# Performance work log

Measured on AMD Instinct MI355X. Metric: run time of the kernel, lower is better.

Reference implementation:

```python
import jax, jax.numpy as jnp
import numpy as np

B, T, D = 4, 2048, 1024
H = 16
HD = D // H  # 64


def setup_inputs() -> dict:
    key = jax.random.key(0)
    k1, k2, k3 = jax.random.split(key, 3)
    x = jax.random.normal(k1, (B, T, D), dtype=jnp.float32)
    w_qkv = jax.random.normal(k2, (D, 3 * D), dtype=jnp.float32) * (1.0 / np.sqrt(D))
    w_out = jax.random.normal(k3, (D, D), dtype=jnp.float32) * (1.0 / np.sqrt(D))
    return {"x": x, "w_qkv": w_qkv, "w_out": w_out}


def reference(x, w_qkv, w_out):
    b, t, c = x.shape
    qkv = x @ w_qkv  # [B,T,3D]
    q, k, v = jnp.split(qkv, 3, axis=-1)

    def heads(u):
        return u.reshape(b, t, H, HD).transpose(0, 2, 1, 3)  # [B,H,T,HD]

    q, k, v = heads(q), heads(k), heads(v)
    scale = 1.0 / np.sqrt(HD).astype(np.float32)
    attn = jnp.einsum('bhqd,bhkd->bhqk', q, k) * scale  # [B,H,T,T]
    causal = jnp.tril(jnp.ones((t, t), dtype=bool))
    attn = jnp.where(causal[None, None, :, :], attn, -jnp.inf)
    attn = jax.nn.softmax(attn, axis=-1)
    y = jnp.einsum('bhqk,bhkd->bhqd', attn, v)  # [B,H,T,HD]
    y = y.transpose(0, 2, 1, 3).reshape(b, t, c)
    return y @ w_out
```

## Files before the change

kernel.cpp:

```cpp
#include <hip/hip_runtime.h>
#include <hip/hip_bf16.h>
#include <stdint.h>

#define B_    4
#define T_    2048
#define D_    1024
#define H_    16
#define HD_   64
#define ROWS_ (B_ * T_)
#define NQKV_ (3 * D_)

typedef __attribute__((ext_vector_type(8))) short bf16x8;
typedef __attribute__((ext_vector_type(4))) float f32x4;

__device__ __forceinline__ unsigned short f2bf(float f) {
    union { float f; uint32_t u; } v; v.f = f;
    uint32_t u = v.u;
    return (unsigned short)((u + 0x7FFFu + ((u >> 16) & 1u)) >> 16);
}

__device__ __forceinline__ uint32_t pack2_rtz(float a, float b) {
    union { float f; uint32_t u; } x, y; x.f = a; y.f = b;
    return (x.u >> 16) | (y.u & 0xFFFF0000u);
}

__device__ __forceinline__ void glds16(const unsigned short* g, unsigned short* l) {
    __builtin_amdgcn_global_load_lds(
        (const __attribute__((address_space(1))) void*)g,
        (__attribute__((address_space(3))) void*)l, 16, 0, 0);
}

__global__ void cvt_bf16_kernel(const float* __restrict__ in,
                                unsigned short* __restrict__ out, int n8) {
    int i = blockIdx.x * blockDim.x + threadIdx.x;
    if (i >= n8) return;
    float4 a = ((const float4*)in)[2 * i];
    float4 b = ((const float4*)in)[2 * i + 1];
    union { bf16x8 v; unsigned short s[8]; } o;
    o.s[0] = f2bf(a.x); o.s[1] = f2bf(a.y); o.s[2] = f2bf(a.z); o.s[3] = f2bf(a.w);
    o.s[4] = f2bf(b.x); o.s[5] = f2bf(b.y); o.s[6] = f2bf(b.z); o.s[7] = f2bf(b.w);
    ((bf16x8*)out)[i] = o.v;
}

__global__ __launch_bounds__(256) void tcvt2_kernel(const float* __restrict__ wqkv,
                                                    const float* __restrict__ wout,
                                                    unsigned short* __restrict__ oqkv,
                                                    unsigned short* __restrict__ oout,
                                                    float scale) {
    __shared__ float tile[64 * 65];
    const int t = threadIdx.x;
    const bool second = blockIdx.x >= 48;
    const float* in = second ? wout : wqkv;
    unsigned short* out = second ? oout : oqkv;
    const int N = second ? 1024 : 3072;
    const int ncut = second ? 0 : 1024;
    const int n0 = (second ? (blockIdx.x - 48) : blockIdx.x) * 64;
    const int k0 = blockIdx.y * 64;
    const int K = 1024;
#pragma unroll
    for (int it = 0; it < 4; ++it) {
        int id = it * 256 + t;
        int r = id >> 4, c = (id & 15) * 4;
        float4 v = *(const float4*)&in[(size_t)(k0 + r) * N + n0 + c];
        tile[r * 65 + c + 0] = v.x; tile[r * 65 + c + 1] = v.y;
        tile[r * 65 + c + 2] = v.z; tile[r * 65 + c + 3] = v.w;
    }
    __syncthreads();
#pragma unroll
    for (int it = 0; it < 2; ++it) {
        int id = it * 256 + t;
        int n = id >> 3, kc = (id & 7) * 8;
        float sc = (n0 + n < ncut) ? scale : 1.0f;
        union { bf16x8 v; unsigned short s[8]; } o;
#pragma unroll
        for (int i = 0; i < 8; ++i) o.s[i] = f2bf(tile[(kc + i) * 65 + n] * sc);
        *(bf16x8*)&out[(size_t)(n0 + n) * K + k0 + kc] = o.v;
    }
}

template<int OUT_BF16, int VSPLIT>
__global__ __launch_bounds__(256) void gemm128_kernel(
    const unsigned short* __restrict__ A,
    const unsigned short* __restrict__ Bt,
    void* __restrict__ Cp, int M, int K, int ldC,
    unsigned short* __restrict__ vt)
{
    __shared__ __align__(16) unsigned short As[128 * 64];
    __shared__ __align__(16) unsigned short Bs[128 * 64];

    const int t = threadIdx.x, w = t >> 6, lane = t & 63;
    const int wm = w >> 1, wn = w & 1;
    const int lm = lane & 15, lq = lane >> 4;
    const int m0 = blockIdx.y * 128, n0 = blockIdx.x * 128;

    f32x4 acc[4][4];
#pragma unroll
    for (int i = 0; i < 4; i++)
#pragma unroll
        for (int j = 0; j < 4; j++) acc[i][j] = (f32x4){0.f, 0.f, 0.f, 0.f};

    const unsigned short* Ap[4];
    const unsigned short* Bp[4];
#pragma unroll
    for (int s = 0; s < 4; s++) {
        int id = s * 256 + t;
        int row = id >> 3, gch = (id & 7) ^ (row & 7);
        Ap[s] = A  + (size_t)(m0 + row) * K + gch * 8;
        Bp[s] = Bt + (size_t)(n0 + row) * K + gch * 8;
    }

    for (int k0 = 0; k0 < K; k0 += 64) {
        __syncthreads();
#pragma unroll
        for (int s = 0; s < 4; s++) glds16(Ap[s] + k0, &As[(s * 256 + t) * 8]);
#pragma unroll
        for (int s = 0; s < 4; s++) glds16(Bp[s] + k0, &Bs[(s * 256 + t) * 8]);
        __syncthreads();

#pragma unroll
        for (int kh = 0; kh < 2; kh++) {
            bf16x8 af[4], bfr[4];
#pragma unroll
            for (int mt = 0; mt < 4; mt++) {
                int row = wm * 64 + mt * 16 + lm;
                int sch = (kh * 4 + lq) ^ (lm & 7);
                af[mt] = *(const bf16x8*)&As[row * 64 + sch * 8];
            }
#pragma unroll
            for (int nt = 0; nt < 4; nt++) {
                int row = wn * 64 + nt * 16 + lm;
                int sch = (kh * 4 + lq) ^ (lm & 7);
                bfr[nt] = *(const bf16x8*)&Bs[row * 64 + sch * 8];
            }
#pragma unroll
            for (int mt = 0; mt < 4; mt++)
#pragma unroll
                for (int nt = 0; nt < 4; nt++)
                    acc[mt][nt] = __builtin_amdgcn_mfma_f32_16x16x32_bf16(
                        af[mt], bfr[nt], acc[mt][nt], 0, 0, 0);
        }
    }

    if (VSPLIT && n0 >= 2048) {
#pragma unroll
        for (int mt = 0; mt < 4; mt++)
#pragma unroll
            for (int nt = 0; nt < 4; nt++) {
                int row0 = m0 + wm * 64 + mt * 16 + lq * 4;
                int col  = n0 + wn * 64 + nt * 16 + lm - 2048;
                int bb = row0 >> 11, tt = row0 & 2047;
                size_t vi = ((size_t)((bb * 16 + (col >> 6)) * 64 + (col & 63))) * 2048 + tt;
                uint2 pk;
                pk.x = (uint32_t)f2bf(acc[mt][nt][0]) | ((uint32_t)f2bf(acc[mt][nt][1]) << 16);
                pk.y = (uint32_t)f2bf(acc[mt][nt][2]) | ((uint32_t)f2bf(acc[mt][nt][3]) << 16);
                *(uint2*)&vt[vi] = pk;
            }
        return;
    }
#pragma unroll
    for (int mt = 0; mt < 4; mt++)
#pragma unroll
        for (int nt = 0; nt < 4; nt++)
#pragma unroll
            for (int r = 0; r < 4; r++) {
                int row = m0 + wm * 64 + mt * 16 + lq * 4 + r;
                int col = n0 + wn * 64 + nt * 16 + lm;
                if (OUT_BF16)
                    ((unsigned short*)Cp)[(size_t)row * ldC + col] = f2bf(acc[mt][nt][r]);
                else
                    ((float*)Cp)[(size_t)row * ldC + col] = acc[mt][nt][r];
            }
}

__global__ __launch_bounds__(256, 4) void attn6_kernel(
    const unsigned short* __restrict__ qk,
    const unsigned short* __restrict__ vt,
    unsigned short* __restrict__ y)
{
    __shared__ __align__(16) unsigned short Ks[64 * 64];
    __shared__ __align__(16) unsigned short Vs[64 * 64];
    __shared__ __align__(16) unsigned short Ps[4][32 * 72];

    const int bh = blockIdx.y;
    const int qt = 15 - blockIdx.x;
    const int b = bh >> 4, h = bh & 15;
    const int t = threadIdx.x, w = t >> 6, lane = t & 63;
    const int lm = lane & 15, lq = lane >> 4;
    unsigned short* psw = Ps[w];

    const int r0 = t >> 3, r1 = r0 + 32, gc = (t & 7) * 8;
    const int xc0 = (((t & 7) ^ (r0 & 7))) * 8;
    const int xc1 = (((t & 7) ^ (r1 & 7))) * 8;
    const unsigned short* kgb = qk + (size_t)(b * T_) * 2048 + D_ + h * HD_;
    const unsigned short* vgb = vt + (size_t)(bh * 64) * 2048;

    const bf16x8 onesf = {0x3F80, 0x3F80, 0x3F80, 0x3F80,
                          0x3F80, 0x3F80, 0x3F80, 0x3F80};

    const int q0 = qt * 128, qw0 = q0 + w * 32;

    bf16x8 qf[2][2];
#pragma unroll
    for (int mt = 0; mt < 2; mt++)
#pragma unroll
        for (int kk = 0; kk < 2; kk++)
            qf[mt][kk] = *(const bf16x8*)
                &qk[(size_t)(b * T_ + qw0 + mt * 16 + lm) * 2048 + h * HD_ + kk * 32 + lq * 8];

    f32x4 o[2][4], osum[2];
#pragma unroll
    for (int mt = 0; mt < 2; mt++) {
        osum[mt] = (f32x4){0.f, 0.f, 0.f, 0.f};
#pragma unroll
        for (int dt = 0; dt < 4; dt++) o[mt][dt] = (f32x4){0.f, 0.f, 0.f, 0.f};
    }

    const int kend = q0 + 128;

    bf16x8 ka = *(const bf16x8*)&kgb[(size_t)r0 * 2048 + gc];
    bf16x8 kb = *(const bf16x8*)&kgb[(size_t)r1 * 2048 + gc];
    bf16x8 va = *(const bf16x8*)&vgb[(size_t)r0 * 2048 + gc];
    bf16x8 vb = *(const bf16x8*)&vgb[(size_t)r1 * 2048 + gc];

    for (int kt = 0; kt < kend; kt += 64) {
        __syncthreads();
        *(bf16x8*)&Ks[r0 * 64 + xc0] = ka;
        *(bf16x8*)&Ks[r1 * 64 + xc1] = kb;
        *(bf16x8*)&Vs[r0 * 64 + xc0] = va;
        *(bf16x8*)&Vs[r1 * 64 + xc1] = vb;
        int ktn = (kt + 64 < kend) ? kt + 64 : kt;
        ka = *(const bf16x8*)&kgb[(size_t)(ktn + r0) * 2048 + gc];
        kb = *(const bf16x8*)&kgb[(size_t)(ktn + r1) * 2048 + gc];
        va = *(const bf16x8*)&vgb[(size_t)r0 * 2048 + ktn + gc];
        vb = *(const bf16x8*)&vgb[(size_t)r1 * 2048 + ktn + gc];
        __syncthreads();
        if (kt >= qw0 + 32) continue;

        f32x4 st[4][2];
#pragma unroll
        for (int nt = 0; nt < 4; nt++)
#pragma unroll
            for (int mt = 0; mt < 2; mt++) st[nt][mt] = (f32x4){0.f, 0.f, 0.f, 0.f};
#pragma unroll
        for (int nt = 0; nt < 4; nt++)
#pragma unroll
            for (int kk = 0; kk < 2; kk++) {
                bf16x8 kf = *(const bf16x8*)
                    &Ks[(nt * 16 + lm) * 64 + ((kk * 4 + lq) ^ (lm & 7)) * 8];
#pragma unroll
                for (int mt = 0; mt < 2; mt++)
                    st[nt][mt] = __builtin_amdgcn_mfma_f32_16x16x32_bf16(
                        kf, qf[mt][kk], st[nt][mt], 0, 0, 0);
            }

        const bool diag = (kt + 64 > qw0);
#pragma unroll
        for (int mt = 0; mt < 2; mt++) {
            const int qi = qw0 + mt * 16 + lm;
#pragma unroll
            for (int nt = 0; nt < 4; nt++) {
                float p[4];
                if (diag) {
                    const int kj0 = kt + nt * 16 + lq * 4;
#pragma unroll
                    for (int r = 0; r < 4; r++)
                        p[r] = (kj0 + r <= qi)
                             ? __builtin_amdgcn_exp2f(st[nt][mt][r]) : 0.f;
                } else {
#pragma unroll
                    for (int r = 0; r < 4; r++)
                        p[r] = __builtin_amdgcn_exp2f(st[nt][mt][r]);
                }
                uint2 pk;
                pk.x = pack2_rtz(p[0], p[1]);
                pk.y = pack2_rtz(p[2], p[3]);
                *(uint2*)&psw[(mt * 16 + lm) * 72 + nt * 16 + lq * 4] = pk;
            }
        }

#pragma unroll
        for (int kk = 0; kk < 2; kk++) {
            bf16x8 pf0 = *(const bf16x8*)&psw[(lm) * 72 + kk * 32 + lq * 8];
            bf16x8 pf1 = *(const bf16x8*)&psw[(16 + lm) * 72 + kk * 32 + lq * 8];
            osum[0] = __builtin_amdgcn_mfma_f32_16x16x32_bf16(pf0, onesf, osum[0], 0, 0, 0);
            osum[1] = __builtin_amdgcn_mfma_f32_16x16x32_bf16(pf1, onesf, osum[1], 0, 0, 0);
#pragma unroll
            for (int dt = 0; dt < 4; dt++) {
                bf16x8 vf = *(const bf16x8*)
                    &Vs[(dt * 16 + lm) * 64 + ((kk * 4 + lq) ^ (lm & 7)) * 8];
                o[0][dt] = __builtin_amdgcn_mfma_f32_16x16x32_bf16(pf0, vf, o[0][dt], 0, 0, 0);
                o[1][dt] = __builtin_amdgcn_mfma_f32_16x16x32_bf16(pf1, vf, o[1][dt], 0, 0, 0);
            }
        }
    }

#pragma unroll
    for (int mt = 0; mt < 2; mt++)
#pragma unroll
        for (int r = 0; r < 4; r++) {
            float rli = 1.f / osum[mt][r];
#pragma unroll
            for (int dt = 0; dt < 4; dt++)
                y[(size_t)(b * T_ + qw0 + mt * 16 + lq * 4 + r) * D_ + h * HD_ + dt * 16 + lm]
                    = f2bf(o[mt][dt][r] * rli);
        }
}

extern "C" void kernel_launch(void* const* d_in, const int* in_sizes, int n_in,
                              void* d_out, int out_size, void* d_ws, size_t ws_size,
                              hipStream_t stream) {
    const float* x    = (const float*)d_in[0];
    const float* wqkv = (const float*)d_in[1];
    const float* wout = (const float*)d_in[2];
    float* out = (float*)d_out;

    char* ws = (char*)d_ws;
    unsigned short* xb     = (unsigned short*)ws; ws += (size_t)ROWS_ * D_ * 2;
    unsigned short* wqkvbt = (unsigned short*)ws; ws += (size_t)D_ * NQKV_ * 2;
    unsigned short* woutbt = (unsigned short*)ws; ws += (size_t)D_ * D_ * 2;
    unsigned short* qkb    = (unsigned short*)ws; ws += (size_t)ROWS_ * 2048 * 2;
    unsigned short* vtb    = (unsigned short*)ws; ws += (size_t)ROWS_ * D_ * 2;
    unsigned short* yb     = (unsigned short*)ws;

    const float SC = 0.18033688011112042f;

    cvt_bf16_kernel<<<ROWS_ * D_ / 8 / 256, 256, 0, stream>>>(x, xb, ROWS_ * D_ / 8);
    tcvt2_kernel<<<dim3(64, 16), 256, 0, stream>>>(wqkv, wout, wqkvbt, woutbt, SC);

    gemm128_kernel<1, 1><<<dim3(NQKV_ / 128, ROWS_ / 128), 256, 0, stream>>>(
        xb, wqkvbt, qkb, ROWS_, D_, 2048, vtb);

    attn6_kernel<<<dim3(16, B_ * H_), 256, 0, stream>>>(qkb, vtb, yb);

    gemm128_kernel<0, 0><<<dim3(D_ / 128, ROWS_ / 128), 256, 0, stream>>>(
        yb, woutbt, out, ROWS_, D_, D_, nullptr);
}
```

Baseline: 272.5 us.

## Pair long and short causal query tiles per block to share K/V loads

```diff
diff --git a/kernel.cpp b/kernel.cpp
--- a/kernel.cpp
+++ b/kernel.cpp
@@ -21,7 +21,7 @@
 
 __device__ __forceinline__ uint32_t pack2_rtz(float a, float b) {
     union { float f; uint32_t u; } x, y; x.f = a; y.f = b;
-    return (x.u >> 16) | (y.u & 0xFFFF0000u);
+    return __builtin_amdgcn_perm(y.u, x.u, 0x07060302u);
 }
 
 __device__ __forceinline__ void glds16(const unsigned short* g, unsigned short* l) {
@@ -151,6 +151,7 @@
                 int bb = row0 >> 11, tt = row0 & 2047;
                 size_t vi = ((size_t)((bb * 16 + (col >> 6)) * 64 + (col & 63))) * 2048 + tt;
                 uint2 pk;
+                pk.x = pack2_rtz(0.f, 0.f);
                 pk.x = (uint32_t)f2bf(acc[mt][nt][0]) | ((uint32_t)f2bf(acc[mt][nt][1]) << 16);
                 pk.y = (uint32_t)f2bf(acc[mt][nt][2]) | ((uint32_t)f2bf(acc[mt][nt][3]) << 16);
                 *(uint2*)&vt[vi] = pk;
@@ -172,7 +173,71 @@
             }
 }
 
-__global__ __launch_bounds__(256, 4) void attn6_kernel(
+__device__ __forceinline__ void attn_step(
+    int kt, int qw0, const bf16x8 (&qf)[2][2],
+    f32x4 (&o)[2][4], f32x4 (&osum)[2],
+    const unsigned short* Ks, const unsigned short* Vs,
+    unsigned short* psw, int lm, int lq, bf16x8 onesf)
+{
+    f32x4 st[4][2];
+#pragma unroll
+    for (int nt = 0; nt < 4; nt++)
+#pragma unroll
+        for (int mt = 0; mt < 2; mt++) st[nt][mt] = (f32x4){0.f, 0.f, 0.f, 0.f};
+#pragma unroll
+    for (int nt = 0; nt < 4; nt++)
+#pragma unroll
+        for (int kk = 0; kk < 2; kk++) {
+            bf16x8 kf = *(const bf16x8*)
+                &Ks[(nt * 16 + lm) * 64 + ((kk * 4 + lq) ^ (lm & 7)) * 8];
+#pragma unroll
+            for (int mt = 0; mt < 2; mt++)
+                st[nt][mt] = __builtin_amdgcn_mfma_f32_16x16x32_bf16(
+                    kf, qf[mt][kk], st[nt][mt], 0, 0, 0);
+        }
+
+    const bool diag = (kt + 64 > qw0);
+#pragma unroll
+    for (int mt = 0; mt < 2; mt++) {
+        const int qi = qw0 + mt * 16 + lm;
+#pragma unroll
+        for (int nt = 0; nt < 4; nt++) {
+            float p[4];
+            if (diag) {
+                const int kj0 = kt + nt * 16 + lq * 4;
+#pragma unroll
+                for (int r = 0; r < 4; r++)
+                    p[r] = (kj0 + r <= qi)
+                         ? __builtin_amdgcn_exp2f(st[nt][mt][r]) : 0.f;
+            } else {
+#pragma unroll
+                for (int r = 0; r < 4; r++)
+                    p[r] = __builtin_amdgcn_exp2f(st[nt][mt][r]);
+            }
+            uint2 pk;
+            pk.x = pack2_rtz(p[0], p[1]);
+            pk.y = pack2_rtz(p[2], p[3]);
+            *(uint2*)&psw[(mt * 16 + lm) * 72 + nt * 16 + lq * 4] = pk;
+        }
+    }
+
+#pragma unroll
+    for (int kk = 0; kk < 2; kk++) {
+        bf16x8 pf0 = *(const bf16x8*)&psw[(lm) * 72 + kk * 32 + lq * 8];
+        bf16x8 pf1 = *(const bf16x8*)&psw[(16 + lm) * 72 + kk * 32 + lq * 8];
+        osum[0] = __builtin_amdgcn_mfma_f32_16x16x32_bf16(pf0, onesf, osum[0], 0, 0, 0);
+        osum[1] = __builtin_amdgcn_mfma_f32_16x16x32_bf16(pf1, onesf, osum[1], 0, 0, 0);
+#pragma unroll
+        for (int dt = 0; dt < 4; dt++) {
+            bf16x8 vf = *(const bf16x8*)
+                &Vs[(dt * 16 + lm) * 64 + ((kk * 4 + lq) ^ (lm & 7)) * 8];
+            o[0][dt] = __builtin_amdgcn_mfma_f32_16x16x32_bf16(pf0, vf, o[0][dt], 0, 0, 0);
+            o[1][dt] = __builtin_amdgcn_mfma_f32_16x16x32_bf16(pf1, vf, o[1][dt], 0, 0, 0);
+        }
+    }
+}
+
+__global__ __launch_bounds__(256) void attn7_kernel(
     const unsigned short* __restrict__ qk,
     const unsigned short* __restrict__ vt,
     unsigned short* __restrict__ y)
@@ -181,128 +246,86 @@
     __shared__ __align__(16) unsigned short Vs[64 * 64];
     __shared__ __align__(16) unsigned short Ps[4][32 * 72];
 
-    const int bh = blockIdx.y;
-    const int qt = 15 - blockIdx.x;
+    const int bh = blockIdx.x, p = blockIdx.y;
     const int b = bh >> 4, h = bh & 15;
     const int t = threadIdx.x, w = t >> 6, lane = t & 63;
     const int lm = lane & 15, lq = lane >> 4;
     unsigned short* psw = Ps[w];
 
     const int r0 = t >> 3, r1 = r0 + 32, gc = (t & 7) * 8;
-    const int xc0 = (((t & 7) ^ (r0 & 7))) * 8;
-    const int xc1 = (((t & 7) ^ (r1 & 7))) * 8;
+    const int xc0 = ((t & 7) ^ (r0 & 7)) * 8;
+    const int xc1 = ((t & 7) ^ (r1 & 7)) * 8;
     const unsigned short* kgb = qk + (size_t)(b * T_) * 2048 + D_ + h * HD_;
     const unsigned short* vgb = vt + (size_t)(bh * 64) * 2048;
 
     const bf16x8 onesf = {0x3F80, 0x3F80, 0x3F80, 0x3F80,
                           0x3F80, 0x3F80, 0x3F80, 0x3F80};
 
-    const int q0 = qt * 128, qw0 = q0 + w * 32;
-
-    bf16x8 qf[2][2];
+    const int qtb = 15 - p, qts = p;
+    const int q0b = qtb * 128, qw0b = q0b + w * 32;
+    const int q0s = qts * 128, qw0s = q0s + w * 32;
+    const int kendb = q0b + 128, kends = q0s + 128;
+
+    bf16x8 qfb[2][2], qfs[2][2];
 #pragma unroll
     for (int mt = 0; mt < 2; mt++)
 #pragma unroll
-        for (int kk = 0; kk < 2; kk++)
-            qf[mt][kk] = *(const bf16x8*)
-                &qk[(size_t)(b * T_ + qw0 + mt * 16 + lm) * 2048 + h * HD_ + kk * 32 + lq * 8];
-
-    f32x4 o[2][4], osum[2];
+        for (int kk = 0; kk < 2; kk++) {
+            qfb[mt][kk] = *(const bf16x8*)
+                &qk[(size_t)(b * T_ + qw0b + mt * 16 + lm) * 2048 + h * HD_ + kk * 32 + lq * 8];
+            qfs[mt][kk] = *(const bf16x8*)
+                &qk[(size_t)(b * T_ + qw0s + mt * 16 + lm) * 2048 + h * HD_ + kk * 32 + lq * 8];
+        }
+
+    f32x4 ob[2][4], osumb[2], os_[2][4], osums[2];
 #pragma unroll
     for (int mt = 0; mt < 2; mt++) {
-        osum[mt] = (f32x4){0.f, 0.f, 0.f, 0.f};
-#pragma unroll
-        for (int dt = 0; dt < 4; dt++) o[mt][dt] = (f32x4){0.f, 0.f, 0.f, 0.f};
-    }
-
-    const int kend = q0 + 128;
+        osumb[mt] = (f32x4){0.f, 0.f, 0.f, 0.f};
+        osums[mt] = (f32x4){0.f, 0.f, 0.f, 0.f};
+#pragma unroll
+        for (int dt = 0; dt < 4; dt++) {
+            ob[mt][dt] = (f32x4){0.f, 0.f, 0.f, 0.f};
+            os_[mt][dt] = (f32x4){0.f, 0.f, 0.f, 0.f};
+        }
+    }
 
     bf16x8 ka = *(const bf16x8*)&kgb[(size_t)r0 * 2048 + gc];
     bf16x8 kb = *(const bf16x8*)&kgb[(size_t)r1 * 2048 + gc];
     bf16x8 va = *(const bf16x8*)&vgb[(size_t)r0 * 2048 + gc];
     bf16x8 vb = *(const bf16x8*)&vgb[(size_t)r1 * 2048 + gc];
 
-    for (int kt = 0; kt < kend; kt += 64) {
+    for (int kt = 0; kt < kendb; kt += 64) {
         __syncthreads();
         *(bf16x8*)&Ks[r0 * 64 + xc0] = ka;
         *(bf16x8*)&Ks[r1 * 64 + xc1] = kb;
         *(bf16x8*)&Vs[r0 * 64 + xc0] = va;
         *(bf16x8*)&Vs[r1 * 64 + xc1] = vb;
-        int ktn = (kt + 64 < kend) ? kt + 64 : kt;
+        int ktn = (kt + 64 < kendb) ? kt + 64 : kt;
         ka = *(const bf16x8*)&kgb[(size_t)(ktn + r0) * 2048 + gc];
         kb = *(const bf16x8*)&kgb[(size_t)(ktn + r1) * 2048 + gc];
         va = *(const bf16x8*)&vgb[(size_t)r0 * 2048 + ktn + gc];
         vb = *(const bf16x8*)&vgb[(size_t)r1 * 2048 + ktn + gc];
         __syncthreads();
-        if (kt >= qw0 + 32) continue;
-
-        f32x4 st[4][2];
-#pragma unroll
-        for (int nt = 0; nt < 4; nt++)
-#pragma unroll
-            for (int mt = 0; mt < 2; mt++) st[nt][mt] = (f32x4){0.f, 0.f, 0.f, 0.f};
-#pragma unroll
-        for (int nt = 0; nt < 4; nt++)
-#pragma unroll
-            for (int kk = 0; kk < 2; kk++) {
-                bf16x8 kf = *(const bf16x8*)
-                    &Ks[(nt * 16 + lm) * 64 + ((kk * 4 + lq) ^ (lm & 7)) * 8];
-#pragma unroll
-                for (int mt = 0; mt < 2; mt++)
-                    st[nt][mt] = __builtin_amdgcn_mfma_f32_16x16x32_bf16(
-                        kf, qf[mt][kk], st[nt][mt], 0, 0, 0);
-            }
-
-        const bool diag = (kt + 64 > qw0);
-#pragma unroll
-        for (int mt = 0; mt < 2; mt++) {
-            const int qi = qw0 + mt * 16 + lm;
-#pragma unroll
-            for (int nt = 0; nt < 4; nt++) {
-                float p[4];
-                if (diag) {
-                    const int kj0 = kt + nt * 16 + lq * 4;
-#pragma unroll
-                    for (int r = 0; r < 4; r++)
-                        p[r] = (kj0 + r <= qi)
-                             ? __builtin_amdgcn_exp2f(st[nt][mt][r]) : 0.f;
-                } else {
-#pragma unroll
-                    for (int r = 0; r < 4; r++)
-                        p[r] = __builtin_amdgcn_exp2f(st[nt][mt][r]);
-                }
-                uint2 pk;
-                pk.x = pack2_rtz(p[0], p[1]);
-                pk.y = pack2_rtz(p[2], p[3]);
-                *(uint2*)&psw[(mt * 16 + lm) * 72 + nt * 16 + lq * 4] = pk;
-            }
-        }
-
-#pragma unroll
-        for (int kk = 0; kk < 2; kk++) {
-            bf16x8 pf0 = *(const bf16x8*)&psw[(lm) * 72 + kk * 32 + lq * 8];
-            bf16x8 pf1 = *(const bf16x8*)&psw[(16 + lm) * 72 + kk * 32 + lq * 8];
-            osum[0] = __builtin_amdgcn_mfma_f32_16x16x32_bf16(pf0, onesf, osum[0], 0, 0, 0);
-            osum[1] = __builtin_amdgcn_mfma_f32_16x16x32_bf16(pf1, onesf, osum[1], 0, 0, 0);
+
+        if (kt < qw0b + 32)
+            attn_step(kt, qw0b, qfb, ob, osumb, Ks, Vs, psw, lm, lq, onesf);
+        if (kt < kends && kt < qw0s + 32)
+            attn_step(kt, qw0s, qfs, os_, osums, Ks, Vs, psw, lm, lq, onesf);
+    }
+
+#pragma unroll
+    for (int mt = 0; mt < 2; mt++)
+#pragma unroll
+        for (int r = 0; r < 4; r++) {
+            float rlb = 1.f / osumb[mt][r];
+            float rls = 1.f / osums[mt][r];
 #pragma unroll
             for (int dt = 0; dt < 4; dt++) {
-                bf16x8 vf = *(const bf16x8*)
-                    &Vs[(dt * 16 + lm) * 64 + ((kk * 4 + lq) ^ (lm & 7)) * 8];
-                o[0][dt] = __builtin_amdgcn_mfma_f32_16x16x32_bf16(pf0, vf, o[0][dt], 0, 0, 0);
-                o[1][dt] = __builtin_amdgcn_mfma_f32_16x16x32_bf16(pf1, vf, o[1][dt], 0, 0, 0);
-            }
-        }
-    }
-
-#pragma unroll
-    for (int mt = 0; mt < 2; mt++)
-#pragma unroll
-        for (int r = 0; r < 4; r++) {
-            float rli = 1.f / osum[mt][r];
-#pragma unroll
-            for (int dt = 0; dt < 4; dt++)
-                y[(size_t)(b * T_ + qw0 + mt * 16 + lq * 4 + r) * D_ + h * HD_ + dt * 16 + lm]
-                    = f2bf(o[mt][dt][r] * rli);
+                y[(size_t)(b * T_ + qw0b + mt * 16 + lq * 4 + r) * D_ + h * HD_ + dt * 16 + lm]
+                    = f2bf(ob[mt][dt][r] * rlb);
+                y[(size_t)(b * T_ + qw0s + mt * 16 + lq * 4 + r) * D_ + h * HD_ + dt * 16 + lm]
+                    = f2bf(os_[mt][dt][r] * rls);
+            }
         }
 }
 
@@ -330,7 +353,7 @@
     gemm128_kernel<1, 1><<<dim3(NQKV_ / 128, ROWS_ / 128), 256, 0, stream>>>(
         xb, wqkvbt, qkb, ROWS_, D_, 2048, vtb);
 
-    attn6_kernel<<<dim3(16, B_ * H_), 256, 0, stream>>>(qkb, vtb, yb);
+    attn7_kernel<<<dim3(B_ * H_, 8), 256, 0, stream>>>(qkb, vtb, yb);
 
     gemm128_kernel<0, 0><<<dim3(D_ / 128, ROWS_ / 128), 256, 0, stream>>>(
         yb, woutbt, out, ROWS_, D_, D_, nullptr);
```

Result: slower. 278.0 us (+2.0%).
